# Performance work log

Measured on AMD Instinct MI355X. Metric: run time of the kernel, lower is better.

## Reference

```python
import jax, jax.numpy as jnp
import numpy as np

S = 7; B = 2; C = 20
IMG_W = 448.0; IMG_H = 448.0
CONF_THRES = 0.5; NMS_THRES = 0.5; IOU_THRES = [0.5]
N = S * S  # 49 boxes per image (one responsible box per cell)
BATCH = 4096


def setup_inputs() -> dict:
    key = jax.random.key(0)
    k1, k2 = jax.random.split(key)
    target = jax.random.uniform(k1, (BATCH, S, S, B * 5 + C), dtype=jnp.float32)
    output = jax.random.normal(k2, (BATCH, S, S, B * 5 + C), dtype=jnp.float32)
    return {"target": target, "output": output}


def _decode(coords):
    # coords: [b,S,S,4] cell-normalized (x,y,w,h) -> xyxy pixel boxes [b,S,S,4]
    gw, gh = IMG_W / S, IMG_H / S
    jx = jnp.arange(S, dtype=coords.dtype)[None, None, :, None]  # column index -> cx
    iy = jnp.arange(S, dtype=coords.dtype)[None, :, None, None]  # row index    -> cy
    cx = (coords[..., 0:1] + jx) * gw
    cy = (coords[..., 1:2] + iy) * gh
    w = coords[..., 2:3] * IMG_W
    h = coords[..., 3:4] * IMG_H
    return jnp.concatenate([cx - w / 2, cy - h / 2, cx + w / 2, cy + h / 2], axis=-1)


def _pairwise_iou(a, b):
    # a: [M,4], b: [K,4] xyxy -> [M,K] IoU (torchvision box_iou semantics)
    lt = jnp.maximum(a[:, None, :2], b[None, :, :2])
    rb = jnp.minimum(a[:, None, 2:], b[None, :, 2:])
    wh = jnp.clip(rb - lt, 0.0)
    inter = wh[..., 0] * wh[..., 1]
    area_a = (a[:, 2] - a[:, 0]) * (a[:, 3] - a[:, 1])
    area_b = (b[:, 2] - b[:, 0]) * (b[:, 3] - b[:, 1])
    return inter / (area_a[:, None] + area_b[None, :] - inter)


def _per_image(ob, oc, ocls, tb, tconf, tcls):
    # Sort preds by conf desc (batched_nms returns score-descending keep order)
    order = jnp.argsort(-oc)
    b_s, c_s, k_s = ob[order], oc[order], ocls[order]
    # class-aware greedy NMS over the 49 boxes
    iou_pp = _pairwise_iou(b_s, b_s)
    sup = (iou_pp > NMS_THRES) & (k_s[:, None] == k_s[None, :])
    idx = jnp.arange(N)
    def nms_body(suppressed, i):
        active = ~suppressed[i]
        suppressed = suppressed | (active & sup[i] & (idx > i))
        return suppressed, active
    _, keep = jax.lax.scan(nms_body, jnp.zeros((N,), bool), idx)
    valid_p = keep & (c_s > CONF_THRES)
    valid_g = tconf > CONF_THRES
    # best same-class GT per pred (max_iou starts at 0 in original; -1 sentinel OK since thr>0)
    cand = (k_s[:, None] == tcls[None, :]) & valid_g[None, :]
    miou = jnp.where(cand, _pairwise_iou(b_s, tb), -1.0)
    return k_s, valid_p, jnp.max(miou, axis=-1), jnp.argmax(miou, axis=-1), valid_g


def _match(mx, best, valid_p, thr):
    # greedy TP/FP assignment over preds in conf-desc order, per image
    def body(matched, i):
        hit = valid_p[i] & (mx[i] > thr) & (~matched[best[i]])
        matched = matched.at[best[i]].set(matched[best[i]] | hit)
        return matched, hit
    _, tp = jax.lax.scan(body, jnp.zeros((N,), bool), jnp.arange(N))
    return tp


def reference(target, output):
    D = B * 5 + C
    target = target.reshape(-1, S, S, D)
    output = jax.nn.sigmoid(output.reshape(-1, S, S, D))
    bsz = output.shape[0]
    # ground-truth decode
    tconf = target[..., 4].reshape(bsz, N)
    tcls = jnp.argmax(target[..., B * 5:], axis=-1).reshape(bsz, N)
    tb = _decode(target[..., 0:4]).reshape(bsz, N, 4)
    # prediction decode: responsible box = max-conf box per cell
    confs = jnp.stack([output[..., b * 5 + 4] for b in range(B)], axis=-1)  # [b,S,S,B]
    oc = jnp.max(confs, axis=-1).reshape(bsz, N)
    resp = jnp.argmax(confs, axis=-1)
    coords = sum((resp == b)[..., None] * output[..., b * 5:b * 5 + 4] for b in range(B))
    ob = _decode(coords).reshape(bsz, N, 4)
    ocls = jnp.argmax(output[..., B * 5:], axis=-1).reshape(bsz, N)

    k_s, valid_p, mx, best, valid_g = jax.vmap(_per_image)(ob, oc, ocls, tb, tconf, tcls)

    # flatten in (image, conf-desc) order == original pred_boxes order
    cls_f = k_s.reshape(-1)
    vp_f = valid_p.reshape(-1)
    gt_count = jax.ops.segment_sum(valid_g.reshape(-1).astype(jnp.float32),
                                   tcls.reshape(-1), num_segments=C)  # [C]
    mask = (cls_f[None, :] == jnp.arange(C)[:, None]) & vp_f[None, :]  # [C, bsz*N]

    aps = []
    for thr in IOU_THRES:
        tp = jax.vmap(_match, in_axes=(0, 0, 0, None))(mx, best, valid_p, thr)
        tp = tp.reshape(-1).astype(jnp.float32)
        # masked entries keep cum values constant -> contribute 0 to trapz
        tpc = jnp.cumsum(jnp.where(mask, tp[None, :], 0.0), axis=1)
        fpc = jnp.cumsum(jnp.where(mask, 1.0 - tp[None, :], 0.0), axis=1)
        recall = tpc / (gt_count[:, None] + 1e-6)
        prec = tpc / (tpc + fpc + 1e-6)
        r = jnp.concatenate([jnp.zeros((C, 1), recall.dtype), recall], axis=1)
        p = jnp.concatenate([jnp.ones((C, 1), prec.dtype), prec], axis=1)
        ap = jnp.sum((r[:, 1:] - r[:, :-1]) * (p[:, 1:] + p[:, :-1]) * 0.5, axis=1)
        has = gt_count > 0  # classes with no GT are skipped in original
        n_has = jnp.maximum(jnp.sum(has.astype(jnp.float32)), 1.0)
        aps.append(jnp.sum(jnp.where(has, ap, 0.0)) / n_has)
    return sum(aps) / len(aps)
```

## Files before the change

kernel.cpp:

```cpp
#include <hip/hip_runtime.h>
#include <stdint.h>

#pragma clang fp contract(off)

#define NCELL 49
#define NCLS  20
#define NSEG  16

struct Box { float x1, y1, x2, y2; };

__device__ __forceinline__ float sigmoid_ref(float x) {
#pragma clang fp contract(off)
  float z = expf(-fabsf(x));
  float num = (x >= 0.0f) ? 1.0f : z;
  return num / (1.0f + z);
}

__device__ __forceinline__ float iou_box(Box a, Box b) {
#pragma clang fp contract(off)
  float lx = fmaxf(a.x1, b.x1);
  float ly = fmaxf(a.y1, b.y1);
  float rx = fminf(a.x2, b.x2);
  float ry = fminf(a.y2, b.y2);
  float w = fmaxf(rx - lx, 0.0f);
  float h = fmaxf(ry - ly, 0.0f);
  float inter = w * h;
  float aa = (a.x2 - a.x1) * (a.y2 - a.y1);
  float ab = (b.x2 - b.x1) * (b.y2 - b.y1);
  return inter / (aa + ab - inter);
}

__device__ __forceinline__ bool iou_gt_half(Box a, Box b) {
#pragma clang fp contract(off)
  float lx = fmaxf(a.x1, b.x1);
  float ly = fmaxf(a.y1, b.y1);
  float rx = fminf(a.x2, b.x2);
  float ry = fminf(a.y2, b.y2);
  float w = fmaxf(rx - lx, 0.0f);
  float h = fmaxf(ry - ly, 0.0f);
  float inter = w * h;
  float aa = (a.x2 - a.x1) * (a.y2 - a.y1);
  float ab = (b.x2 - b.x1) * (b.y2 - b.y1);
  float u = aa + ab - inter;
  return inter > 0.5f * u;
}

__device__ __forceinline__ unsigned mbcnt64(unsigned long long m) {
  return __builtin_amdgcn_mbcnt_hi((unsigned)(m >> 32),
         __builtin_amdgcn_mbcnt_lo((unsigned)m, 0u));
}
#define WSYNC() __builtin_amdgcn_wave_barrier()

__global__ __launch_bounds__(128) void k_per_image(
    const float* __restrict__ target, const float* __restrict__ output,
    uint8_t* __restrict__ entries, unsigned* __restrict__ gtseg,
    unsigned* __restrict__ totals, int batch, int segimg)
{
#pragma clang fp contract(off)
  __shared__ float4   pbox [2][64];
  __shared__ int2     pcc  [2][64];
  __shared__ float4   gboxC[2][64];
  __shared__ int      gorig[2][64];
  __shared__ float    ctab [2][64];
  __shared__ int      claim[2][64];
  __shared__ unsigned phist[2][NCLS];

  int tid = threadIdx.x;
  int lane = tid & 63;
  int wv = tid >> 6;
  int img = blockIdx.x * 2 + wv;
  if (img >= batch) return;
  bool a = (lane < NCELL);
  int seg = img / segimg;

  if (lane < NCLS) phist[wv][lane] = 0u;
  claim[wv][lane] = 64;

  float fjx = (float)(lane % 7), fiy = (float)(lane / 7);

  float ov[30], tv[30];
  if (a) {
    const float2* O2 = (const float2*)(output + (size_t)img * 1470 + lane * 30);
    const float2* T2 = (const float2*)(target + (size_t)img * 1470 + lane * 30);
#pragma unroll
    for (int i = 0; i < 15; ++i) { float2 o = O2[i]; ov[2*i] = o.x; ov[2*i+1] = o.y; }
#pragma unroll
    for (int i = 0; i < 15; ++i) { float2 t = T2[i]; tv[2*i] = t.x; tv[2*i+1] = t.y; }
  } else {
#pragma unroll
    for (int i = 0; i < 30; ++i) { ov[i] = 0.0f; tv[i] = 0.0f; }
  }

  {
    float myc = -1.0f; int myk = 0; float px1 = 0, py1 = 0, px2 = 0, py2 = 0;
    if (a) {
      float x4 = ov[4], x9 = ov[9];
      float xm = fmaxf(x4, x9);
      float xc = ov[10], xr = -3.0e38f; int kk = 0;
#pragma unroll
      for (int c = 1; c < NCLS; ++c) {
        float v = ov[10 + c];
        bool gt = v > xc;
        float nr = gt ? xc : fmaxf(xr, v);
        kk = gt ? c : kk;
        xc = gt ? v : xc;
        xr = nr;
      }
      bool slowK = (xc - xr) < fmaxf(1e-5f, 4e-6f * exp2f(xc * 1.44269504f));
      bool slowR = fabsf(x4 - x9) < fmaxf(1e-5f, 4e-6f * exp2f(xm * 1.44269504f));
      int resp = (x9 > x4) ? 1 : 0;
      myc = sigmoid_ref(xm);
      myk = kk;
      if (slowK || slowR) {
        float s0 = sigmoid_ref(x4);
        float s1 = sigmoid_ref(x9);
        myc = fmaxf(s0, s1);
        resp = (s1 > s0) ? 1 : 0;
        float obv = sigmoid_ref(ov[10]); myk = 0;
#pragma unroll
        for (int c = 1; c < NCLS; ++c) {
          float v = sigmoid_ref(ov[10 + c]);
          if (v > obv) { obv = v; myk = c; }
        }
      }
      float bx = resp ? ov[5] : ov[0];
      float by = resp ? ov[6] : ov[1];
      float bw = resp ? ov[7] : ov[2];
      float bh = resp ? ov[8] : ov[3];
      float x  = sigmoid_ref(bx);
      float y  = sigmoid_ref(by);
      float ww = sigmoid_ref(bw);
      float hh = sigmoid_ref(bh);
      float cx = (x + fjx) * 64.0f, cy = (y + fiy) * 64.0f;
      float W = ww * 448.0f, H = hh * 448.0f;
      px1 = cx - W * 0.5f; py1 = cy - H * 0.5f;
      px2 = cx + W * 0.5f; py2 = cy + H * 0.5f;
    }
    ctab[wv][lane] = myc;
    WSYNC();
    int r = 0;
#pragma unroll
    for (int j = 0; j < NCELL; ++j) {
      float cj = ctab[wv][j];
      r += (cj > myc) || (cj == myc && j < lane);
    }
    r = a ? r : lane;
    pbox[wv][r] = make_float4(px1, py1, px2, py2);
    pcc [wv][r] = make_int2(myk, __float_as_int(myc));
  }

  int mystartR = 0, myendR = 0;
  unsigned gcnt_mine = 0;
  int gclsv = 0; bool gval = false;
  float4 gb4;
  {
    float tbv = tv[10];
#pragma unroll
    for (int c = 1; c < NCLS; ++c) { float v = tv[10 + c]; if (v > tbv) { tbv = v; gclsv = c; } }
    gval = a && (tv[4] > 0.5f);
    float cx = (tv[0] + fjx) * 64.0f, cy = (tv[1] + fiy) * 64.0f;
    float w2 = tv[2] * 448.0f, h2 = tv[3] * 448.0f;
    gb4 = make_float4(cx - w2 * 0.5f, cy - h2 * 0.5f,
                      cx + w2 * 0.5f, cy + h2 * 0.5f);
  }

  WSYNC();
  float4 sb4 = pbox[wv][lane];
  int2 cc = pcc[wv][lane];
  Box myS; myS.x1 = sb4.x; myS.y1 = sb4.y; myS.x2 = sb4.z; myS.y2 = sb4.w;
  int scls = cc.x; float sconf = __int_as_float(cc.y);

  {
    int base = 0, mypos = -1;
#pragma unroll
    for (int c = 0; c < NCLS; ++c) {
      unsigned long long mc = __ballot(gval && (gclsv == c));
      int cnt = (int)__popcll(mc);
      if (scls == c) { mystartR = base; myendR = base + cnt; }
      if (gval && gclsv == c) mypos = base + (int)mbcnt64(mc);
      if (lane == c) gcnt_mine = (unsigned)cnt;
      base += cnt;
    }
    if (mypos >= 0) {
      gboxC[wv][mypos] = gb4;
      gorig[wv][mypos] = lane;
    }
    if (lane < NCLS && gcnt_mine) atomicAdd(&gtseg[seg * 32 + lane], gcnt_mine);
  }
  if (!a) { mystartR = 0; myendR = 0; }
  WSYNC();

  float mx = -1.0f; int best = 0;
  for (int g = mystartR; g < myendR; ++g) {
    float4 b4 = gboxC[wv][g];
    int og = gorig[wv][g];
    Box bg; bg.x1 = b4.x; bg.y1 = b4.y; bg.x2 = b4.z; bg.y2 = b4.w;
    float v = iou_box(myS, bg);
    bool upd = (v > mx);
    mx = upd ? v : mx;
    best = upd ? og : best;
  }

  unsigned long long row = 0;
#pragma unroll 4
  for (int t = 1; t <= 24; ++t) {
    int jr = lane + t;
    bool wrapped = (jr >= 49);
    int j = wrapped ? jr - 49 : jr;
    float4 b4 = pbox[wv][j];
    int kj = pcc[wv][j].x;
    Box bj; bj.x1 = b4.x; bj.y1 = b4.y; bj.x2 = b4.z; bj.y2 = b4.w;
    bool s = a && (scls == kj) && iou_gt_half(myS, bj);
    row |= (s && !wrapped) ? (1ull << (jr & 63)) : 0ull;
    unsigned long long m2 = __ballot(s && wrapped);
    int idx = lane + 49 - t;
    unsigned long long bit = (m2 >> (idx & 63)) & 1ull;
    row |= (idx < 49) ? (bit << (idx & 63)) : 0ull;
  }
  unsigned long long anyrow = __ballot(row != 0ull);
  unsigned supbit = 0u;
  while (anyrow) {
    int i = (int)__builtin_ctzll(anyrow);
    anyrow &= anyrow - 1;
    unsigned long long ri = __shfl(row, i, 64);
    unsigned si = __shfl(supbit, i, 64);
    supbit |= (!si && ((ri >> lane) & 1ull)) ? 1u : 0u;
  }
  bool vp = a && (supbit == 0u) && (sconf > 0.5f);

  bool elig = vp && (mx > 0.5f);
  if (elig) atomicMin(&claim[wv][best], lane);
  WSYNC();
  bool hit = elig && (claim[wv][best] == lane);

  if (a) {
    entries[(size_t)img * NCELL + lane] =
        (uint8_t)(scls | (vp ? 32 : 0) | (hit ? 64 : 0));
  }

  unsigned add = (vp ? 0x10000u : 0u) | (hit ? 1u : 0u);
  if (a && add) atomicAdd(&phist[wv][scls], add);
  WSYNC();
  if (lane < NCLS) {
    unsigned pkt = phist[wv][lane];
    if (pkt) atomicAdd(&totals[seg * 32 + lane], pkt);
  }
}

__device__ __forceinline__ unsigned match_mask(unsigned w, unsigned wantx4) {
  unsigned y = (w & 0x3f3f3f3fu) ^ wantx4;
  return ~(y + 0x7f7f7f7fu) & 0x80808080u;
}

__device__ __forceinline__ uint4 load_tile(const uint8_t* entries, int e, int e1, int ne) {
  uint4 w4 = make_uint4(0, 0, 0, 0);
  if (e < e1) {
    int p = e << 4;
    if (p + 16 <= ne) {
      w4 = *(const uint4*)(entries + p);
    } else {
      unsigned ws[4] = {0, 0, 0, 0};
      for (int k = 0; k < ne - p; ++k)
        ws[k >> 2] |= ((unsigned)entries[p + k]) << (8 * (k & 3));
      w4.x = ws[0]; w4.y = ws[1]; w4.z = ws[2]; w4.w = ws[3];
    }
  }
  return w4;
}

__global__ __launch_bounds__(1024) void k_apB_fast(
    const uint8_t* __restrict__ entries, const unsigned* __restrict__ totals,
    const unsigned* __restrict__ gtseg, double* __restrict__ partials,
    unsigned* __restrict__ counter, float* __restrict__ out,
    int ne, int segimg)
{
#pragma clang fp contract(off)
  int c = blockIdx.x / NSEG, s = blockIdx.x % NSEG;
  int tid = threadIdx.x, wid = tid >> 6, lane = tid & 63;
  unsigned gtc = 0;
#pragma unroll
  for (int s2 = 0; s2 < NSEG; ++s2) gtc += gtseg[s2 * 32 + c];
  float g2 = (float)gtc + 1e-6f;
  unsigned wantx4 = (32u + (unsigned)c) * 0x01010101u;

  int nel = (ne + 15) >> 4;
  int segel = segimg * NCELL / 16;
  int se0 = s * segel; if (se0 > nel) se0 = nel;
  int se1 = se0 + segel; if (se1 > nel) se1 = nel;
  int elw = (se1 > se0) ? ((se1 - se0 + 15) >> 4) : 0;
  int e0 = se0 + wid * elw; if (e0 > se1) e0 = se1;
  int e1 = e0 + elw; if (e1 > se1) e1 = se1;

  unsigned long long pk = 0;
  if (lane < s) {
    unsigned t2 = totals[lane * 32 + c];
    pk = ((unsigned long long)(t2 >> 16) << 32) | (unsigned long long)(t2 & 0xffffu);
  }
#pragma unroll
  for (int d = 1; d < 64; d <<= 1) pk += __shfl_xor(pk, d, 64);
  unsigned Jrun = (unsigned)(pk >> 32), Trun = (unsigned)(pk & 0xffffffffull);

  int e = e0 + lane;
  int p = e << 4;
  uint4 w4 = load_tile(entries, e, e1, ne);
  unsigned wsv[4] = {w4.x, w4.y, w4.z, w4.w};
  unsigned mm[4], tm[4];
  unsigned cv = 0, ct = 0;
#pragma unroll
  for (int q = 0; q < 4; ++q) {
    unsigned m = match_mask(wsv[q], wantx4);
    mm[q] = m; tm[q] = m & (wsv[q] << 1);
    cv += __popc(m); ct += __popc(tm[q]);
  }

  unsigned long long tot = ((unsigned long long)cv << 32) | (unsigned long long)ct;
#pragma unroll
  for (int d = 1; d < 64; d <<= 1) tot += __shfl_xor(tot, d, 64);
  __shared__ unsigned long long wt[16];
  __shared__ double wacc[16];
  __shared__ int islast;
  __shared__ float apf_s[NCLS];
  __shared__ unsigned ghas_s[NCLS];
  if (lane == 0) wt[wid] = tot;
  __syncthreads();
  for (int w2 = 0; w2 < wid; ++w2) {
    Jrun += (unsigned)(wt[w2] >> 32);
    Trun += (unsigned)(wt[w2] & 0xffffffffull);
  }

  unsigned jexcl = 0, texcl = 0;
#pragma unroll
  for (int b = 0; b < 5; ++b) {
    unsigned long long mj = __ballot(((cv >> b) & 1u) != 0u);
    unsigned long long mk = __ballot(((ct >> b) & 1u) != 0u);
    jexcl += mbcnt64(mj) << b;
    texcl += mbcnt64(mk) << b;
  }
  unsigned jr = Jrun + jexcl;
  unsigned tr = Trun + texcl;

  double acc = 0.0;
#pragma unroll
  for (int q = 0; q < 4; ++q) {
    unsigned m = mm[q];
    while (m) {
      unsigned bit = (unsigned)__builtin_ctz(m);
      m &= m - 1;
      ++jr;
      if (tm[q] & (1u << bit)) {
        ++tr;
        int pos = p + 4 * q + (int)(bit >> 3);
        float ft = (float)tr, fj = (float)jr;
        float r_cur  = ft / g2;
        float r_prev = (ft - 1.0f) / g2;
        float p_cur  = ft / (fj + 1e-6f);
        float p_prev = (pos == 0) ? 1.0f
                                  : (ft - 1.0f) / ((fj - 1.0f) + 1e-6f);
        acc += (double)((r_cur - r_prev) * (p_cur + p_prev) * 0.5f);
      }
    }
  }

  for (int d = 32; d > 0; d >>= 1) acc += __shfl_down(acc, d, 64);
  if (lane == 0) wacc[wid] = acc;
  __syncthreads();
  if (tid == 0) {
    double bp = 0.0;
#pragma unroll
    for (int w2 = 0; w2 < 16; ++w2) bp += wacc[w2];
    __hip_atomic_store(&partials[blockIdx.x], bp,
                       __ATOMIC_RELEASE, __HIP_MEMORY_SCOPE_AGENT);
    unsigned prev = __hip_atomic_fetch_add(counter, 1u,
                       __ATOMIC_ACQ_REL, __HIP_MEMORY_SCOPE_AGENT);
    islast = (prev == (unsigned)(NCLS * NSEG - 1)) ? 1 : 0;
  }
  __syncthreads();
  if (islast) {
    if (tid < NCLS) {
      double d2 = 0.0;
#pragma unroll
      for (int s2 = 0; s2 < NSEG; ++s2)
        d2 += __hip_atomic_load(&partials[tid * NSEG + s2],
                                __ATOMIC_ACQUIRE, __HIP_MEMORY_SCOPE_AGENT);
      apf_s[tid] = (float)d2;
      unsigned gc = 0;
#pragma unroll
      for (int s2 = 0; s2 < NSEG; ++s2) gc += gtseg[s2 * 32 + tid];
      ghas_s[tid] = gc;
    }
    __syncthreads();
    if (tid == 0) {
      float sf = 0.0f, nf = 0.0f;
      for (int cc = 0; cc < NCLS; ++cc)
        if (ghas_s[cc] > 0) { sf += apf_s[cc]; nf += 1.0f; }
      out[0] = sf / fmaxf(nf, 1.0f);
    }
  }
}

__global__ __launch_bounds__(256) void k_apB(
    const uint8_t* __restrict__ entries, const unsigned* __restrict__ totals,
    const unsigned* __restrict__ gtseg, double* __restrict__ partials,
    unsigned* __restrict__ counter, float* __restrict__ out,
    int ne, int segimg)
{
#pragma clang fp contract(off)
  int c = blockIdx.x / NSEG, s = blockIdx.x % NSEG;
  int tid = threadIdx.x, wid = tid >> 6, lane = tid & 63;
  unsigned gtc = 0;
#pragma unroll
  for (int s2 = 0; s2 < NSEG; ++s2) gtc += gtseg[s2 * 32 + c];
  float g2 = (float)gtc + 1e-6f;
  unsigned wantx4 = (32u + (unsigned)c) * 0x01010101u;

  int nel = (ne + 15) >> 4;
  int segel = segimg * NCELL / 16;
  int se0 = s * segel; if (se0 > nel) se0 = nel;
  int se1 = se0 + segel; if (se1 > nel) se1 = nel;
  int elw = (se1 > se0) ? ((se1 - se0 + 3) >> 2) : 0;
  int e0 = se0 + wid * elw; if (e0 > se1) e0 = se1;
  int e1 = e0 + elw; if (e1 > se1) e1 = se1;
  int ntile = (e1 > e0) ? ((e1 - e0 + 63) >> 6) : 0;

  unsigned long long pk = 0;
  if (lane < s) {
    unsigned t2 = totals[lane * 32 + c];
    pk = ((unsigned long long)(t2 >> 16) << 32) | (unsigned long long)(t2 & 0xffffu);
  }
#pragma unroll
  for (int d = 1; d < 64; d <<= 1) pk += __shfl_xor(pk, d, 64);
  unsigned Jrun = (unsigned)(pk >> 32), Trun = (unsigned)(pk & 0xffffffffull);

  unsigned mv = 0, mt = 0;
  for (int t = 0; t < ntile; ++t) {
    uint4 w4 = load_tile(entries, e0 + t * 64 + lane, e1, ne);
    unsigned wsv[4] = {w4.x, w4.y, w4.z, w4.w};
#pragma unroll
    for (int q = 0; q < 4; ++q) {
      unsigned m = match_mask(wsv[q], wantx4);
      mv += __popc(m);
      mt += __popc(m & (wsv[q] << 1));
    }
  }
  unsigned long long tot = ((unsigned long long)mv << 32) | (unsigned long long)mt;
#pragma unroll
  for (int d = 1; d < 64; d <<= 1) tot += __shfl_xor(tot, d, 64);
  __shared__ unsigned long long wt[4];
  __shared__ double wacc[4];
  __shared__ int islast;
  __shared__ float apf_s[NCLS];
  __shared__ unsigned ghas_s[NCLS];
  if (lane == 0) wt[wid] = tot;
  __syncthreads();
  for (int w2 = 0; w2 < wid; ++w2) {
    Jrun += (unsigned)(wt[w2] >> 32);
    Trun += (unsigned)(wt[w2] & 0xffffffffull);
  }

  double acc = 0.0;
  for (int t = 0; t < ntile; ++t) {
    int e = e0 + t * 64 + lane;
    int p = e << 4;
    uint4 w4 = load_tile(entries, e, e1, ne);
    unsigned wsv[4] = {w4.x, w4.y, w4.z, w4.w};
    unsigned mm[4], tm[4];
    unsigned cv = 0, ct = 0;
#pragma unroll
    for (int q = 0; q < 4; ++q) {
      unsigned m = match_mask(wsv[q], wantx4);
      mm[q] = m; tm[q] = m & (wsv[q] << 1);
      cv += __popc(m); ct += __popc(tm[q]);
    }
    unsigned jexcl = 0, texcl = 0, jtt = 0, ttt = 0;
#pragma unroll
    for (int b = 0; b < 5; ++b) {
      unsigned long long mj = __ballot(((cv >> b) & 1u) != 0u);
      unsigned long long mk = __ballot(((ct >> b) & 1u) != 0u);
      jexcl += mbcnt64(mj) << b;
      texcl += mbcnt64(mk) << b;
      jtt   += (unsigned)__popcll(mj) << b;
      ttt   += (unsigned)__popcll(mk) << b;
    }
    unsigned jr = Jrun + jexcl;
    unsigned tr = Trun + texcl;
#pragma unroll
    for (int q = 0; q < 4; ++q) {
      unsigned m = mm[q];
      while (m) {
        unsigned bit = (unsigned)__builtin_ctz(m);
        m &= m - 1;
        ++jr;
        if (tm[q] & (1u << bit)) {
          ++tr;
          int pos = p + 4 * q + (int)(bit >> 3);
          float ft = (float)tr, fj = (float)jr;
          float r_cur  = ft / g2;
          float r_prev = (ft - 1.0f) / g2;
          float p_cur  = ft / (fj + 1e-6f);
          float p_prev = (pos == 0) ? 1.0f
                                    : (ft - 1.0f) / ((fj - 1.0f) + 1e-6f);
          acc += (double)((r_cur - r_prev) * (p_cur + p_prev) * 0.5f);
        }
      }
    }
    Jrun += jtt;
    Trun += ttt;
  }

  for (int d = 32; d > 0; d >>= 1) acc += __shfl_down(acc, d, 64);
  if (lane == 0) wacc[wid] = acc;
  __syncthreads();
  if (tid == 0) {
    double bp = wacc[0] + wacc[1] + wacc[2] + wacc[3];
    __hip_atomic_store(&partials[blockIdx.x], bp,
                       __ATOMIC_RELEASE, __HIP_MEMORY_SCOPE_AGENT);
    unsigned prev = __hip_atomic_fetch_add(counter, 1u,
                       __ATOMIC_ACQ_REL, __HIP_MEMORY_SCOPE_AGENT);
    islast = (prev == (unsigned)(NCLS * NSEG - 1)) ? 1 : 0;
  }
  __syncthreads();
  if (islast) {
    if (tid < NCLS) {
      double d2 = 0.0;
#pragma unroll
      for (int s2 = 0; s2 < NSEG; ++s2)
        d2 += __hip_atomic_load(&partials[tid * NSEG + s2],
                                __ATOMIC_ACQUIRE, __HIP_MEMORY_SCOPE_AGENT);
      apf_s[tid] = (float)d2;
      unsigned gc = 0;
#pragma unroll
      for (int s2 = 0; s2 < NSEG; ++s2) gc += gtseg[s2 * 32 + tid];
      ghas_s[tid] = gc;
    }
    __syncthreads();
    if (tid == 0) {
      float sf = 0.0f, nf = 0.0f;
      for (int cc = 0; cc < NCLS; ++cc)
        if (ghas_s[cc] > 0) { sf += apf_s[cc]; nf += 1.0f; }
      out[0] = sf / fmaxf(nf, 1.0f);
    }
  }
}

extern "C" void kernel_launch(void* const* d_in, const int* in_sizes, int n_in,
                              void* d_out, int out_size, void* d_ws, size_t ws_size,
                              hipStream_t stream) {
  const float* target = (const float*)d_in[0];
  const float* output = (const float*)d_in[1];
  int batch = in_sizes[0] / (NCELL * 30);
  int ne = batch * NCELL;
  int segimg = (((batch + NSEG - 1) / NSEG) + 15) & ~15;

  uint8_t*  entries  = (uint8_t*)d_ws;
  size_t offA = ((size_t)ne + 255) & ~(size_t)255;
  unsigned* totals   = (unsigned*)((char*)d_ws + offA);
  unsigned* gtseg    = (unsigned*)((char*)d_ws + offA + 2048);
  unsigned* counter  = (unsigned*)((char*)d_ws + offA + 4096);
  double*   partials = (double*)((char*)d_ws + offA + 4352);

  (void)hipMemsetAsync((char*)d_ws + offA, 0, 4352, stream);
  k_per_image<<<(batch + 1) / 2, 128, 0, stream>>>(
      target, output, entries, gtseg, totals, batch, segimg);
  int segel = segimg * NCELL / 16;
  if (segel <= 1024) {
    k_apB_fast<<<NCLS * NSEG, 1024, 0, stream>>>(
        entries, totals, gtseg, partials, counter, (float*)d_out, ne, segimg);
  } else {
    k_apB<<<NCLS * NSEG, 256, 0, stream>>>(
        entries, totals, gtseg, partials, counter, (float*)d_out, ne, segimg);
  }
}
```

Baseline: 116.4 us.

## Fuse per-image and AP kernels into one launch with a spin-wait on completion

Merges the per-image NMS/matching kernel and the AP accumulation kernel into a single launch. The trailing blocks spin on a global done counter before reading the entries. The AP blocks are reshaped from 1024 threads to 128 threads, each handling up to 8 tiles. The goal is to remove a kernel launch boundary and its drain/fill gap. The risk is deadlock if the AP blocks occupy CUs before all image blocks get scheduled; the guard on total block count only partly mitigates this, and the spinning blocks waste slots.

```diff
diff --git a/kernel.cpp b/kernel.cpp
--- a/kernel.cpp
+++ b/kernel.cpp
@@ -51,6 +51,372 @@
 }
 #define WSYNC() __builtin_amdgcn_wave_barrier()
 
+__device__ __forceinline__ unsigned match_mask(unsigned w, unsigned wantx4) {
+  unsigned y = (w & 0x3f3f3f3fu) ^ wantx4;
+  return ~(y + 0x7f7f7f7fu) & 0x80808080u;
+}
+
+__device__ __forceinline__ uint4 load_tile(const uint8_t* entries, int e, int e1, int ne) {
+  uint4 w4 = make_uint4(0, 0, 0, 0);
+  if (e < e1) {
+    int p = e << 4;
+    if (p + 16 <= ne) {
+      w4 = *(const uint4*)(entries + p);
+    } else {
+      unsigned ws[4] = {0, 0, 0, 0};
+      for (int k = 0; k < ne - p; ++k)
+        ws[k >> 2] |= ((unsigned)entries[p + k]) << (8 * (k & 3));
+      w4.x = ws[0]; w4.y = ws[1]; w4.z = ws[2]; w4.w = ws[3];
+    }
+  }
+  return w4;
+}
+
+__global__ __launch_bounds__(128, 5) void k_fused(
+    const float* __restrict__ target, const float* __restrict__ output,
+    uint8_t* __restrict__ entries, unsigned* __restrict__ gtseg,
+    unsigned* __restrict__ totals, unsigned* __restrict__ done,
+    double* __restrict__ partials, unsigned* __restrict__ counter2,
+    float* __restrict__ out, int batch, int segimg, int nimgb, int ne)
+{
+#pragma clang fp contract(off)
+  __shared__ float4   pbox [2][64];
+  __shared__ int2     pcc  [2][64];
+  __shared__ float4   gboxC[2][64];
+  __shared__ int      gorig[2][64];
+  __shared__ float    ctab [2][64];
+  __shared__ int      claim[2][64];
+  __shared__ unsigned phist[2][NCLS];
+  __shared__ unsigned long long awt[2];
+  __shared__ double   awacc[2];
+  __shared__ int      islast;
+  __shared__ float    apf_s[NCLS];
+  __shared__ unsigned ghas_s[NCLS];
+
+  int tid = threadIdx.x;
+  int lane = tid & 63;
+  int wv = tid >> 6;
+  int bid = blockIdx.x;
+
+  if (bid < nimgb) {
+    int img = bid * 2 + wv;
+    bool act = (img < batch);
+    if (act) {
+      bool a = (lane < NCELL);
+      int seg = img / segimg;
+
+      if (lane < NCLS) phist[wv][lane] = 0u;
+      claim[wv][lane] = 64;
+
+      float fjx = (float)(lane % 7), fiy = (float)(lane / 7);
+
+      float ov[30], tv[30];
+      if (a) {
+        const float2* O2 = (const float2*)(output + (size_t)img * 1470 + lane * 30);
+        const float2* T2 = (const float2*)(target + (size_t)img * 1470 + lane * 30);
+#pragma unroll
+        for (int i = 0; i < 15; ++i) { float2 o = O2[i]; ov[2*i] = o.x; ov[2*i+1] = o.y; }
+#pragma unroll
+        for (int i = 0; i < 15; ++i) { float2 t = T2[i]; tv[2*i] = t.x; tv[2*i+1] = t.y; }
+      } else {
+#pragma unroll
+        for (int i = 0; i < 30; ++i) { ov[i] = 0.0f; tv[i] = 0.0f; }
+      }
+
+      {
+        float myc = -1.0f; int myk = 0; float px1 = 0, py1 = 0, px2 = 0, py2 = 0;
+        if (a) {
+          float x4 = ov[4], x9 = ov[9];
+          float xm = fmaxf(x4, x9);
+          float xc = ov[10], xr = -3.0e38f; int kk = 0;
+#pragma unroll
+          for (int c = 1; c < NCLS; ++c) {
+            float v = ov[10 + c];
+            bool gt = v > xc;
+            float nr = gt ? xc : fmaxf(xr, v);
+            kk = gt ? c : kk;
+            xc = gt ? v : xc;
+            xr = nr;
+          }
+          bool slowK = (xc - xr) < fmaxf(1e-5f, 4e-6f * exp2f(xc * 1.44269504f));
+          bool slowR = fabsf(x4 - x9) < fmaxf(1e-5f, 4e-6f * exp2f(xm * 1.44269504f));
+          int resp = (x9 > x4) ? 1 : 0;
+          myc = sigmoid_ref(xm);
+          myk = kk;
+          if (slowK || slowR) {
+            float s0 = sigmoid_ref(x4);
+            float s1 = sigmoid_ref(x9);
+            myc = fmaxf(s0, s1);
+            resp = (s1 > s0) ? 1 : 0;
+            float obv = sigmoid_ref(ov[10]); myk = 0;
+#pragma unroll
+            for (int c = 1; c < NCLS; ++c) {
+              float v = sigmoid_ref(ov[10 + c]);
+              if (v > obv) { obv = v; myk = c; }
+            }
+          }
+          float bx = resp ? ov[5] : ov[0];
+          float by = resp ? ov[6] : ov[1];
+          float bw = resp ? ov[7] : ov[2];
+          float bh = resp ? ov[8] : ov[3];
+          float x  = sigmoid_ref(bx);
+          float y  = sigmoid_ref(by);
+          float ww = sigmoid_ref(bw);
+          float hh = sigmoid_ref(bh);
+          float cx = (x + fjx) * 64.0f, cy = (y + fiy) * 64.0f;
+          float W = ww * 448.0f, H = hh * 448.0f;
+          px1 = cx - W * 0.5f; py1 = cy - H * 0.5f;
+          px2 = cx + W * 0.5f; py2 = cy + H * 0.5f;
+        }
+        ctab[wv][lane] = myc;
+        WSYNC();
+        int r = 0;
+#pragma unroll
+        for (int j = 0; j < NCELL; ++j) {
+          float cj = ctab[wv][j];
+          r += (cj > myc) || (cj == myc && j < lane);
+        }
+        r = a ? r : lane;
+        pbox[wv][r] = make_float4(px1, py1, px2, py2);
+        pcc [wv][r] = make_int2(myk, __float_as_int(myc));
+      }
+
+      int mystartR = 0, myendR = 0;
+      unsigned gcnt_mine = 0;
+      int gclsv = 0; bool gval = false;
+      float4 gb4;
+      {
+        float tbv = tv[10];
+#pragma unroll
+        for (int c = 1; c < NCLS; ++c) { float v = tv[10 + c]; if (v > tbv) { tbv = v; gclsv = c; } }
+        gval = a && (tv[4] > 0.5f);
+        float cx = (tv[0] + fjx) * 64.0f, cy = (tv[1] + fiy) * 64.0f;
+        float w2 = tv[2] * 448.0f, h2 = tv[3] * 448.0f;
+        gb4 = make_float4(cx - w2 * 0.5f, cy - h2 * 0.5f,
+                          cx + w2 * 0.5f, cy + h2 * 0.5f);
+      }
+
+      WSYNC();
+      float4 sb4 = pbox[wv][lane];
+      int2 cc = pcc[wv][lane];
+      Box myS; myS.x1 = sb4.x; myS.y1 = sb4.y; myS.x2 = sb4.z; myS.y2 = sb4.w;
+      int scls = cc.x; float sconf = __int_as_float(cc.y);
+
+      {
+        int base = 0, mypos = -1;
+#pragma unroll
+        for (int c = 0; c < NCLS; ++c) {
+          unsigned long long mc = __ballot(gval && (gclsv == c));
+          int cnt = (int)__popcll(mc);
+          if (scls == c) { mystartR = base; myendR = base + cnt; }
+          if (gval && gclsv == c) mypos = base + (int)mbcnt64(mc);
+          if (lane == c) gcnt_mine = (unsigned)cnt;
+          base += cnt;
+        }
+        if (mypos >= 0) {
+          gboxC[wv][mypos] = gb4;
+          gorig[wv][mypos] = lane;
+        }
+        if (lane < NCLS && gcnt_mine) atomicAdd(&gtseg[seg * 32 + lane], gcnt_mine);
+      }
+      if (!a) { mystartR = 0; myendR = 0; }
+      WSYNC();
+
+      float mx = -1.0f; int best = 0;
+      for (int g = mystartR; g < myendR; ++g) {
+        float4 b4 = gboxC[wv][g];
+        int og = gorig[wv][g];
+        Box bg; bg.x1 = b4.x; bg.y1 = b4.y; bg.x2 = b4.z; bg.y2 = b4.w;
+        float v = iou_box(myS, bg);
+        bool upd = (v > mx);
+        mx = upd ? v : mx;
+        best = upd ? og : best;
+      }
+
+      unsigned long long row = 0;
+#pragma unroll 4
+      for (int t = 1; t <= 24; ++t) {
+        int jr2 = lane + t;
+        bool wrapped = (jr2 >= 49);
+        int j = wrapped ? jr2 - 49 : jr2;
+        float4 b4 = pbox[wv][j];
+        int kj = pcc[wv][j].x;
+        Box bj; bj.x1 = b4.x; bj.y1 = b4.y; bj.x2 = b4.z; bj.y2 = b4.w;
+        bool s = a && (scls == kj) && iou_gt_half(myS, bj);
+        row |= (s && !wrapped) ? (1ull << (jr2 & 63)) : 0ull;
+        unsigned long long m2 = __ballot(s && wrapped);
+        int idx = lane + 49 - t;
+        unsigned long long bit = (m2 >> (idx & 63)) & 1ull;
+        row |= (idx < 49) ? (bit << (idx & 63)) : 0ull;
+      }
+      unsigned long long anyrow = __ballot(row != 0ull);
+      unsigned supbit = 0u;
+      while (anyrow) {
+        int i = (int)__builtin_ctzll(anyrow);
+        anyrow &= anyrow - 1;
+        unsigned long long ri = __shfl(row, i, 64);
+        unsigned si = __shfl(supbit, i, 64);
+        supbit |= (!si && ((ri >> lane) & 1ull)) ? 1u : 0u;
+      }
+      bool vp = a && (supbit == 0u) && (sconf > 0.5f);
+
+      bool elig = vp && (mx > 0.5f);
+      if (elig) atomicMin(&claim[wv][best], lane);
+      WSYNC();
+      bool hit = elig && (claim[wv][best] == lane);
+
+      if (a) {
+        entries[(size_t)img * NCELL + lane] =
+            (uint8_t)(scls | (vp ? 32 : 0) | (hit ? 64 : 0));
+      }
+
+      unsigned add = (vp ? 0x10000u : 0u) | (hit ? 1u : 0u);
+      if (a && add) atomicAdd(&phist[wv][scls], add);
+      WSYNC();
+      if (lane < NCLS) {
+        unsigned pkt = phist[wv][lane];
+        if (pkt) atomicAdd(&totals[seg * 32 + lane], pkt);
+      }
+    }
+    __syncthreads();
+    if (tid == 0) {
+      __threadfence();
+      __hip_atomic_fetch_add(done, 1u, __ATOMIC_RELEASE, __HIP_MEMORY_SCOPE_AGENT);
+    }
+  } else {
+    int u = bid - nimgb;
+    int c = u / NSEG, s = u % NSEG;
+    unsigned wantx4 = (32u + (unsigned)c) * 0x01010101u;
+    int nel = (ne + 15) >> 4;
+    int segel = segimg * NCELL / 16;
+    int se0 = s * segel; if (se0 > nel) se0 = nel;
+    int se1 = se0 + segel; if (se1 > nel) se1 = nel;
+    int navail = se1 - se0;
+    int rl = (navail + 127) >> 7;
+    int li = tid;
+    int myE0 = se0 + li * rl; if (myE0 > se1) myE0 = se1;
+    int myE1 = myE0 + rl; if (myE1 > se1) myE1 = se1;
+
+    if (tid == 0) {
+      while (__hip_atomic_load(done, __ATOMIC_ACQUIRE, __HIP_MEMORY_SCOPE_AGENT)
+             < (unsigned)nimgb)
+        __builtin_amdgcn_s_sleep(16);
+    }
+    __syncthreads();
+
+    unsigned gtc = 0;
+#pragma unroll
+    for (int s2 = 0; s2 < NSEG; ++s2) gtc += gtseg[s2 * 32 + c];
+    float g2 = (float)gtc + 1e-6f;
+
+    uint4 w4s[8];
+#pragma unroll
+    for (int t = 0; t < 8; ++t)
+      w4s[t] = (t < rl) ? load_tile(entries, myE0 + t, myE1, ne)
+                        : make_uint4(0, 0, 0, 0);
+
+    unsigned cv = 0, ct = 0;
+#pragma unroll
+    for (int t = 0; t < 8; ++t) {
+      unsigned wsv[4] = {w4s[t].x, w4s[t].y, w4s[t].z, w4s[t].w};
+#pragma unroll
+      for (int q = 0; q < 4; ++q) {
+        unsigned m = match_mask(wsv[q], wantx4);
+        cv += __popc(m);
+        ct += __popc(m & (wsv[q] << 1));
+      }
+    }
+
+    unsigned long long pv = ((unsigned long long)cv << 32) | (unsigned long long)ct;
+    unsigned long long scan = pv;
+#pragma unroll
+    for (int d = 1; d < 64; d <<= 1) {
+      unsigned long long o = __shfl_up(scan, d, 64);
+      if (lane >= d) scan += o;
+    }
+    unsigned long long wtot = __shfl(scan, 63, 64);
+    if (lane == 0) awt[wv] = wtot;
+    __syncthreads();
+    unsigned long long excl = scan - pv;
+    if (wv == 1) excl += awt[0];
+
+    unsigned long long pk = 0;
+    if (lane < s) {
+      unsigned t2 = totals[lane * 32 + c];
+      pk = ((unsigned long long)(t2 >> 16) << 32) | (unsigned long long)(t2 & 0xffffu);
+    }
+#pragma unroll
+    for (int d = 1; d < 64; d <<= 1) pk += __shfl_xor(pk, d, 64);
+
+    unsigned jr = (unsigned)(pk >> 32) + (unsigned)(excl >> 32);
+    unsigned tr = (unsigned)(pk & 0xffffffffull) + (unsigned)(excl & 0xffffffffull);
+
+    double acc = 0.0;
+#pragma unroll
+    for (int t = 0; t < 8; ++t) {
+      if (t < rl && (myE0 + t) < myE1) {
+        int p = (myE0 + t) << 4;
+        unsigned wsv[4] = {w4s[t].x, w4s[t].y, w4s[t].z, w4s[t].w};
+#pragma unroll
+        for (int q = 0; q < 4; ++q) {
+          unsigned m = match_mask(wsv[q], wantx4);
+          unsigned tm = m & (wsv[q] << 1);
+          while (m) {
+            unsigned bit = (unsigned)__builtin_ctz(m);
+            m &= m - 1;
+            ++jr;
+            if (tm & (1u << bit)) {
+              ++tr;
+              int pos = p + 4 * q + (int)(bit >> 3);
+              float ft = (float)tr, fj = (float)jr;
+              float r_cur  = ft / g2;
+              float r_prev = (ft - 1.0f) / g2;
+              float p_cur  = ft / (fj + 1e-6f);
+              float p_prev = (pos == 0) ? 1.0f
+                                        : (ft - 1.0f) / ((fj - 1.0f) + 1e-6f);
+              acc += (double)((r_cur - r_prev) * (p_cur + p_prev) * 0.5f);
+            }
+          }
+        }
+      }
+    }
+
+    for (int d = 32; d > 0; d >>= 1) acc += __shfl_down(acc, d, 64);
+    if (lane == 0) awacc[wv] = acc;
+    __syncthreads();
+    if (tid == 0) {
+      double bp = awacc[0] + awacc[1];
+      __hip_atomic_store(&partials[u], bp,
+                         __ATOMIC_RELEASE, __HIP_MEMORY_SCOPE_AGENT);
+      unsigned prev = __hip_atomic_fetch_add(counter2, 1u,
+                         __ATOMIC_ACQ_REL, __HIP_MEMORY_SCOPE_AGENT);
+      islast = (prev == (unsigned)(NCLS * NSEG - 1)) ? 1 : 0;
+    }
+    __syncthreads();
+    if (islast) {
+      if (tid < NCLS) {
+        double d2 = 0.0;
+#pragma unroll
+        for (int s2 = 0; s2 < NSEG; ++s2)
+          d2 += __hip_atomic_load(&partials[tid * NSEG + s2],
+                                  __ATOMIC_ACQUIRE, __HIP_MEMORY_SCOPE_AGENT);
+        apf_s[tid] = (float)d2;
+        unsigned gc = 0;
+#pragma unroll
+        for (int s2 = 0; s2 < NSEG; ++s2) gc += gtseg[s2 * 32 + tid];
+        ghas_s[tid] = gc;
+      }
+      __syncthreads();
+      if (tid == 0) {
+        float sf = 0.0f, nf = 0.0f;
+        for (int cc2 = 0; cc2 < NCLS; ++cc2)
+          if (ghas_s[cc2] > 0) { sf += apf_s[cc2]; nf += 1.0f; }
+        out[0] = sf / fmaxf(nf, 1.0f);
+      }
+    }
+  }
+}
+
 __global__ __launch_bounds__(128) void k_per_image(
     const float* __restrict__ target, const float* __restrict__ output,
     uint8_t* __restrict__ entries, unsigned* __restrict__ gtseg,
@@ -204,14 +570,14 @@
   unsigned long long row = 0;
 #pragma unroll 4
   for (int t = 1; t <= 24; ++t) {
-    int jr = lane + t;
-    bool wrapped = (jr >= 49);
-    int j = wrapped ? jr - 49 : jr;
+    int jr2 = lane + t;
+    bool wrapped = (jr2 >= 49);
+    int j = wrapped ? jr2 - 49 : jr2;
     float4 b4 = pbox[wv][j];
     int kj = pcc[wv][j].x;
     Box bj; bj.x1 = b4.x; bj.y1 = b4.y; bj.x2 = b4.z; bj.y2 = b4.w;
     bool s = a && (scls == kj) && iou_gt_half(myS, bj);
-    row |= (s && !wrapped) ? (1ull << (jr & 63)) : 0ull;
+    row |= (s && !wrapped) ? (1ull << (jr2 & 63)) : 0ull;
     unsigned long long m2 = __ballot(s && wrapped);
     int idx = lane + 49 - t;
     unsigned long long bit = (m2 >> (idx & 63)) & 1ull;
@@ -244,157 +610,6 @@
   if (lane < NCLS) {
     unsigned pkt = phist[wv][lane];
     if (pkt) atomicAdd(&totals[seg * 32 + lane], pkt);
-  }
-}
-
-__device__ __forceinline__ unsigned match_mask(unsigned w, unsigned wantx4) {
-  unsigned y = (w & 0x3f3f3f3fu) ^ wantx4;
-  return ~(y + 0x7f7f7f7fu) & 0x80808080u;
-}
-
-__device__ __forceinline__ uint4 load_tile(const uint8_t* entries, int e, int e1, int ne) {
-  uint4 w4 = make_uint4(0, 0, 0, 0);
-  if (e < e1) {
-    int p = e << 4;
-    if (p + 16 <= ne) {
-      w4 = *(const uint4*)(entries + p);
-    } else {
-      unsigned ws[4] = {0, 0, 0, 0};
-      for (int k = 0; k < ne - p; ++k)
-        ws[k >> 2] |= ((unsigned)entries[p + k]) << (8 * (k & 3));
-      w4.x = ws[0]; w4.y = ws[1]; w4.z = ws[2]; w4.w = ws[3];
-    }
-  }
-  return w4;
-}
-
-__global__ __launch_bounds__(1024) void k_apB_fast(
-    const uint8_t* __restrict__ entries, const unsigned* __restrict__ totals,
-    const unsigned* __restrict__ gtseg, double* __restrict__ partials,
-    unsigned* __restrict__ counter, float* __restrict__ out,
-    int ne, int segimg)
-{
-#pragma clang fp contract(off)
-  int c = blockIdx.x / NSEG, s = blockIdx.x % NSEG;
-  int tid = threadIdx.x, wid = tid >> 6, lane = tid & 63;
-  unsigned gtc = 0;
-#pragma unroll
-  for (int s2 = 0; s2 < NSEG; ++s2) gtc += gtseg[s2 * 32 + c];
-  float g2 = (float)gtc + 1e-6f;
-  unsigned wantx4 = (32u + (unsigned)c) * 0x01010101u;
-
-  int nel = (ne + 15) >> 4;
-  int segel = segimg * NCELL / 16;
-  int se0 = s * segel; if (se0 > nel) se0 = nel;
-  int se1 = se0 + segel; if (se1 > nel) se1 = nel;
-  int elw = (se1 > se0) ? ((se1 - se0 + 15) >> 4) : 0;
-  int e0 = se0 + wid * elw; if (e0 > se1) e0 = se1;
-  int e1 = e0 + elw; if (e1 > se1) e1 = se1;
-
-  unsigned long long pk = 0;
-  if (lane < s) {
-    unsigned t2 = totals[lane * 32 + c];
-    pk = ((unsigned long long)(t2 >> 16) << 32) | (unsigned long long)(t2 & 0xffffu);
-  }
-#pragma unroll
-  for (int d = 1; d < 64; d <<= 1) pk += __shfl_xor(pk, d, 64);
-  unsigned Jrun = (unsigned)(pk >> 32), Trun = (unsigned)(pk & 0xffffffffull);
-
-  int e = e0 + lane;
-  int p = e << 4;
-  uint4 w4 = load_tile(entries, e, e1, ne);
-  unsigned wsv[4] = {w4.x, w4.y, w4.z, w4.w};
-  unsigned mm[4], tm[4];
-  unsigned cv = 0, ct = 0;
-#pragma unroll
-  for (int q = 0; q < 4; ++q) {
-    unsigned m = match_mask(wsv[q], wantx4);
-    mm[q] = m; tm[q] = m & (wsv[q] << 1);
-    cv += __popc(m); ct += __popc(tm[q]);
-  }
-
-  unsigned long long tot = ((unsigned long long)cv << 32) | (unsigned long long)ct;
-#pragma unroll
-  for (int d = 1; d < 64; d <<= 1) tot += __shfl_xor(tot, d, 64);
-  __shared__ unsigned long long wt[16];
-  __shared__ double wacc[16];
-  __shared__ int islast;
-  __shared__ float apf_s[NCLS];
-  __shared__ unsigned ghas_s[NCLS];
-  if (lane == 0) wt[wid] = tot;
-  __syncthreads();
-  for (int w2 = 0; w2 < wid; ++w2) {
-    Jrun += (unsigned)(wt[w2] >> 32);
-    Trun += (unsigned)(wt[w2] & 0xffffffffull);
-  }
-
-  unsigned jexcl = 0, texcl = 0;
-#pragma unroll
-  for (int b = 0; b < 5; ++b) {
-    unsigned long long mj = __ballot(((cv >> b) & 1u) != 0u);
-    unsigned long long mk = __ballot(((ct >> b) & 1u) != 0u);
-    jexcl += mbcnt64(mj) << b;
-    texcl += mbcnt64(mk) << b;
-  }
-  unsigned jr = Jrun + jexcl;
-  unsigned tr = Trun + texcl;
-
-  double acc = 0.0;
-#pragma unroll
-  for (int q = 0; q < 4; ++q) {
-    unsigned m = mm[q];
-    while (m) {
-      unsigned bit = (unsigned)__builtin_ctz(m);
-      m &= m - 1;
-      ++jr;
-      if (tm[q] & (1u << bit)) {
-        ++tr;
-        int pos = p + 4 * q + (int)(bit >> 3);
-        float ft = (float)tr, fj = (float)jr;
-        float r_cur  = ft / g2;
-        float r_prev = (ft - 1.0f) / g2;
-        float p_cur  = ft / (fj + 1e-6f);
-        float p_prev = (pos == 0) ? 1.0f
-                                  : (ft - 1.0f) / ((fj - 1.0f) + 1e-6f);
-        acc += (double)((r_cur - r_prev) * (p_cur + p_prev) * 0.5f);
-      }
-    }
-  }
-
-  for (int d = 32; d > 0; d >>= 1) acc += __shfl_down(acc, d, 64);
-  if (lane == 0) wacc[wid] = acc;
-  __syncthreads();
-  if (tid == 0) {
-    double bp = 0.0;
-#pragma unroll
-    for (int w2 = 0; w2 < 16; ++w2) bp += wacc[w2];
-    __hip_atomic_store(&partials[blockIdx.x], bp,
-                       __ATOMIC_RELEASE, __HIP_MEMORY_SCOPE_AGENT);
-    unsigned prev = __hip_atomic_fetch_add(counter, 1u,
-                       __ATOMIC_ACQ_REL, __HIP_MEMORY_SCOPE_AGENT);
-    islast = (prev == (unsigned)(NCLS * NSEG - 1)) ? 1 : 0;
-  }
-  __syncthreads();
-  if (islast) {
-    if (tid < NCLS) {
-      double d2 = 0.0;
-#pragma unroll
-      for (int s2 = 0; s2 < NSEG; ++s2)
-        d2 += __hip_atomic_load(&partials[tid * NSEG + s2],
-                                __ATOMIC_ACQUIRE, __HIP_MEMORY_SCOPE_AGENT);
-      apf_s[tid] = (float)d2;
-      unsigned gc = 0;
-#pragma unroll
-      for (int s2 = 0; s2 < NSEG; ++s2) gc += gtseg[s2 * 32 + tid];
-      ghas_s[tid] = gc;
-    }
-    __syncthreads();
-    if (tid == 0) {
-      float sf = 0.0f, nf = 0.0f;
-      for (int cc = 0; cc < NCLS; ++cc)
-        if (ghas_s[cc] > 0) { sf += apf_s[cc]; nf += 1.0f; }
-      out[0] = sf / fmaxf(nf, 1.0f);
-    }
   }
 }
 
@@ -555,18 +770,24 @@
   size_t offA = ((size_t)ne + 255) & ~(size_t)255;
   unsigned* totals   = (unsigned*)((char*)d_ws + offA);
   unsigned* gtseg    = (unsigned*)((char*)d_ws + offA + 2048);
-  unsigned* counter  = (unsigned*)((char*)d_ws + offA + 4096);
-  double*   partials = (double*)((char*)d_ws + offA + 4352);
-
-  (void)hipMemsetAsync((char*)d_ws + offA, 0, 4352, stream);
-  k_per_image<<<(batch + 1) / 2, 128, 0, stream>>>(
-      target, output, entries, gtseg, totals, batch, segimg);
+  unsigned* done     = (unsigned*)((char*)d_ws + offA + 4096);
+  unsigned* counter2 = (unsigned*)((char*)d_ws + offA + 4100);
+  double*   partials = (double*)((char*)d_ws + offA + 4608);
+
+  (void)hipMemsetAsync((char*)d_ws + offA, 0, 4608, stream);
+
+  int nimgb = (batch + 1) / 2;
   int segel = segimg * NCELL / 16;
-  if (segel <= 1024) {
-    k_apB_fast<<<NCLS * NSEG, 1024, 0, stream>>>(
-        entries, totals, gtseg, partials, counter, (float*)d_out, ne, segimg);
+  int rl = (segel + 127) >> 7;
+  bool fused_ok = (rl <= 8) && (nimgb + NCLS * NSEG <= 2560);
+  if (fused_ok) {
+    k_fused<<<nimgb + NCLS * NSEG, 128, 0, stream>>>(
+        target, output, entries, gtseg, totals, done, partials, counter2,
+        (float*)d_out, batch, segimg, nimgb, ne);
   } else {
+    k_per_image<<<nimgb, 128, 0, stream>>>(
+        target, output, entries, gtseg, totals, batch, segimg);
     k_apB<<<NCLS * NSEG, 256, 0, stream>>>(
-        entries, totals, gtseg, partials, counter, (float*)d_out, ne, segimg);
-  }
-}
+        entries, totals, gtseg, partials, counter2, (float*)d_out, ne, segimg);
+  }
+}
```

Result: slower. 207.8 us (+78.6%).
